# Kernel optimization log

Measured on AMD Instinct MI355X. Metric: run time of the kernel, lower is better.

## Reference

```python
import jax, jax.numpy as jnp
import numpy as np


def setup_inputs() -> dict:
    key = jax.random.key(0)
    k1, k2 = jax.random.split(key)
    N, M, D = 8192, 8192, 512
    x = jax.random.normal(k1, (N, D), dtype=jnp.float32)
    y = jax.random.normal(k2, (M, D), dtype=jnp.float32)
    gamma = jnp.float32(1.0)
    return {"x": x, "y": y, "gamma": gamma}


def reference(x, y, gamma):
    # k(x, y) = exp(-gamma * ||x - y||^2)
    x = x.reshape(-1, x.shape[-1])
    y = y.reshape(-1, y.shape[-1])
    x_sq = jnp.sum(x * x, axis=-1)  # [N]
    y_sq = jnp.sum(y * y, axis=-1)  # [M]
    cross = x @ y.T                  # [N, M]
    sq_dist = x_sq[:, None] + y_sq[None, :] - 2.0 * cross
    sq_dist = jnp.maximum(sq_dist, 0.0)  # guard tiny negative roundoff
    return jnp.exp(-gamma * sq_dist)
```

## Files before the change

kernel.cpp:

```cpp
#include <hip/hip_runtime.h>
#include <hip/hip_bf16.h>

typedef unsigned short u16;
typedef __attribute__((ext_vector_type(8))) short bf16x8;
typedef __attribute__((ext_vector_type(4))) float f32x4;

typedef const __attribute__((address_space(1))) void gvoid_t;
typedef __attribute__((address_space(3))) void lvoid_t;

__device__ __forceinline__ void gload_lds16(const void* g, void* l) {
  __builtin_amdgcn_global_load_lds((gvoid_t*)g, (lvoid_t*)l, 16, 0, 0);
}

__device__ __forceinline__ u16 f2bf(float f) {
  union { float f; unsigned u; } a;
  a.f = f;
  unsigned r = (a.u + 0x7FFFu + ((a.u >> 16) & 1u)) >> 16;
  return (u16)r;
}

__global__ __launch_bounds__(128) void rbf_prep(
    const float* __restrict__ x, const float* __restrict__ y,
    u16* __restrict__ xb, u16* __restrict__ yb,
    float* __restrict__ xsq, float* __restrict__ ysq,
    int N, int M, int D) {
  int row = blockIdx.x;
  const float* src;
  u16* dst;
  float* sq;
  if (row < N) {
    src = x + (size_t)row * D;
    dst = xb + (size_t)row * D;
    sq = xsq + row;
  } else {
    int r = row - N;
    src = y + (size_t)r * D;
    dst = yb + (size_t)r * D;
    sq = ysq + r;
  }
  int t = threadIdx.x;
  float4 v = reinterpret_cast<const float4*>(src)[t];
  float s = v.x * v.x + v.y * v.y + v.z * v.z + v.w * v.w;
  ushort4 o;
  o.x = f2bf(v.x);
  o.y = f2bf(v.y);
  o.z = f2bf(v.z);
  o.w = f2bf(v.w);
  reinterpret_cast<ushort4*>(dst)[t] = o;
  #pragma unroll
  for (int off = 32; off > 0; off >>= 1) s += __shfl_down(s, off, 64);
  __shared__ float red[2];
  if ((t & 63) == 0) red[t >> 6] = s;
  __syncthreads();
  if (t == 0) sq[0] = red[0] + red[1];
}

#define BM 256
#define BN 256
#define BK 64

__global__ __launch_bounds__(512, 2) void rbf_gemm(
    const u16* __restrict__ xb, const u16* __restrict__ yb,
    const float* __restrict__ xsq, const float* __restrict__ ysq,
    const float* __restrict__ gptr, float* __restrict__ out,
    int N, int M, int D) {
  __shared__ u16 lds[2][2][BM * BK];

  int nwg = gridDim.x;
  int bid = blockIdx.x;
  int cpx = nwg >> 3;
  int swz = (bid & 7) * cpx + (bid >> 3);
  int nbn = M / BN;
  int brow = (swz / nbn) * BM;
  int bcol = (swz % nbn) * BN;

  int tid = threadIdx.x;
  int w = tid >> 6;
  int lane = tid & 63;
  int wm = w >> 2;
  int wn = w & 3;
  int fr = lane & 15;
  int fq = lane >> 4;

  int srow = lane >> 3;
  int scol = ((lane & 7) * 8) ^ ((lane >= 32) ? 16 : 0);
  const u16* xsrc = xb + (size_t)(brow + w * 32 + srow) * D + scol;
  const u16* ysrc = yb + (size_t)(bcol + w * 32 + srow) * D + scol;
  int sdst = w * 4 * 512;

  int cswz = (fr & 4) ? 16 : 0;
  int colx0 = (fq * 8) ^ cswz;
  int colx1 = (32 + fq * 8) ^ cswz;
  int aoff0 = (wm * 128 + fr) * 64 + colx0;
  int aoff1 = (wm * 128 + fr) * 64 + colx1;
  int boff0 = (wn * 64 + fr) * 64 + colx0;
  int boff1 = (wn * 64 + fr) * 64 + colx1;

  f32x4 acc[8][4];
  #pragma unroll
  for (int m = 0; m < 8; ++m)
    #pragma unroll
    for (int n = 0; n < 4; ++n)
      acc[m][n] = (f32x4){0.f, 0.f, 0.f, 0.f};

  auto stage = [&](int kt, int b) {
    const u16* xs = xsrc + kt * 64;
    const u16* ys = ysrc + kt * 64;
    u16* la = &lds[b][0][sdst];
    u16* lb = &lds[b][1][sdst];
    #pragma unroll
    for (int i = 0; i < 4; ++i)
      gload_lds16(xs + (size_t)i * 8 * D, la + i * 512);
    #pragma unroll
    for (int i = 0; i < 4; ++i)
      gload_lds16(ys + (size_t)i * 8 * D, lb + i * 512);
  };

#define PHASE(MH, NH, RA, RB)                                                  \
  {                                                                            \
    if (RA) {                                                                  \
      _Pragma("unroll") for (int mi = 0; mi < 4; ++mi) {                       \
        af[mi][0] = *(const bf16x8*)&A[aoff0 + (MH * 4 + mi) * 1024];          \
        af[mi][1] = *(const bf16x8*)&A[aoff1 + (MH * 4 + mi) * 1024];          \
      }                                                                        \
    }                                                                          \
    if (RB) {                                                                  \
      _Pragma("unroll") for (int ni = 0; ni < 2; ++ni) {                       \
        bf[ni][0] = *(const bf16x8*)&B[boff0 + (NH * 2 + ni) * 1024];          \
        bf[ni][1] = *(const bf16x8*)&B[boff1 + (NH * 2 + ni) * 1024];          \
      }                                                                        \
    }                                                                          \
    __builtin_amdgcn_s_setprio(1);                                             \
    _Pragma("unroll") for (int mi = 0; mi < 4; ++mi)                           \
      _Pragma("unroll") for (int ni = 0; ni < 2; ++ni) {                       \
        acc[MH * 4 + mi][NH * 2 + ni] =                                        \
            __builtin_amdgcn_mfma_f32_16x16x32_bf16(                           \
                af[mi][0], bf[ni][0], acc[MH * 4 + mi][NH * 2 + ni], 0, 0, 0); \
        acc[MH * 4 + mi][NH * 2 + ni] =                                        \
            __builtin_amdgcn_mfma_f32_16x16x32_bf16(                           \
                af[mi][1], bf[ni][1], acc[MH * 4 + mi][NH * 2 + ni], 0, 0, 0); \
      }                                                                        \
    __builtin_amdgcn_s_setprio(0);                                             \
  }

  int nkt = D >> 6;
  stage(0, 0);
  stage(1, 1);
  for (int t = 0; t < nkt; ++t) {
    int b = t & 1;
    if (t + 1 < nkt)
      asm volatile("s_waitcnt vmcnt(8)" ::: "memory");
    else
      asm volatile("s_waitcnt vmcnt(0)" ::: "memory");
    __builtin_amdgcn_sched_barrier(0);
    __builtin_amdgcn_s_barrier();
    __builtin_amdgcn_sched_barrier(0);

    const u16* A = &lds[b][0][0];
    const u16* B = &lds[b][1][0];
    bf16x8 af[4][2], bf[2][2];

    PHASE(0, 0, true, true);
    __builtin_amdgcn_s_barrier();
    PHASE(0, 1, false, true);
    __builtin_amdgcn_s_barrier();
    PHASE(1, 1, true, false);
    __builtin_amdgcn_s_barrier();
    PHASE(1, 0, false, true);

    asm volatile("s_waitcnt lgkmcnt(0)" ::: "memory");
    __builtin_amdgcn_sched_barrier(0);
    __builtin_amdgcn_s_barrier();
    __builtin_amdgcn_sched_barrier(0);
    if (t + 2 < nkt) stage(t + 2, b);
  }
#undef PHASE

  float gamma = gptr[0];
  float ysv[4];
  #pragma unroll
  for (int n = 0; n < 4; ++n) ysv[n] = ysq[bcol + wn * 64 + n * 16 + fr];
  #pragma unroll
  for (int m = 0; m < 8; ++m) {
    #pragma unroll
    for (int r = 0; r < 4; ++r) {
      int i = brow + wm * 128 + m * 16 + fq * 4 + r;
      float xs = xsq[i];
      size_t ro = (size_t)i * M;
      #pragma unroll
      for (int n = 0; n < 4; ++n) {
        int j = bcol + wn * 64 + n * 16 + fr;
        float d2 = fmaxf(xs + ysv[n] - 2.0f * acc[m][n][r], 0.0f);
        out[ro + j] = __expf(-gamma * d2);
      }
    }
  }
}

__global__ __launch_bounds__(256) void rbf_naive(
    const float* __restrict__ x, const float* __restrict__ y,
    const float* __restrict__ gptr, float* __restrict__ out,
    int N, int M, int D) {
  __shared__ float xs[16][17];
  __shared__ float ys[16][17];
  int nbn = M / 16;
  int brow = (blockIdx.x / nbn) * 16;
  int bcol = (blockIdx.x % nbn) * 16;
  int ti = threadIdx.x >> 4, tj = threadIdx.x & 15;
  float dacc = 0.f, xacc = 0.f, yacc = 0.f;
  for (int k0 = 0; k0 < D; k0 += 16) {
    xs[ti][tj] = x[(size_t)(brow + ti) * D + k0 + tj];
    ys[ti][tj] = y[(size_t)(bcol + ti) * D + k0 + tj];
    __syncthreads();
    #pragma unroll
    for (int kk = 0; kk < 16; ++kk) {
      float xv = xs[ti][kk], yv = ys[tj][kk];
      dacc += xv * yv;
      xacc += xv * xv;
      yacc += yv * yv;
    }
    __syncthreads();
  }
  float gamma = gptr[0];
  float d2 = fmaxf(xacc + yacc - 2.f * dacc, 0.f);
  out[(size_t)(brow + ti) * M + (bcol + tj)] = __expf(-gamma * d2);
}

extern "C" void kernel_launch(void* const* d_in, const int* in_sizes, int n_in,
                              void* d_out, int out_size, void* d_ws,
                              size_t ws_size, hipStream_t stream) {
  const float* x = (const float*)d_in[0];
  const float* y = (const float*)d_in[1];
  const float* g = (const float*)d_in[2];
  float* out = (float*)d_out;

  const int D = 512;
  const int N = in_sizes[0] / D;
  const int M = in_sizes[1] / D;

  size_t need = (size_t)(N + M) * D * sizeof(u16) + (size_t)(N + M) * sizeof(float);
  bool shapes_ok = (N % BM == 0) && (M % BN == 0) && (D % BK == 0) && (D / BK >= 2);

  if (ws_size >= need && shapes_ok) {
    u16* xb = (u16*)d_ws;
    u16* yb = xb + (size_t)N * D;
    float* xsq = (float*)(yb + (size_t)M * D);
    float* ysq = xsq + N;

    rbf_prep<<<N + M, 128, 0, stream>>>(x, y, xb, yb, xsq, ysq, N, M, D);
    int nwg = (N / BM) * (M / BN);
    rbf_gemm<<<nwg, 512, 0, stream>>>(xb, yb, xsq, ysq, g, out, N, M, D);
  } else {
    rbf_naive<<<(N / 16) * (M / 16), 256, 0, stream>>>(x, y, g, out, N, M, D);
  }
}
```

Measured before the change: 124.5 us.

## Use full XOR LDS swizzle and transposed MFMA operands for vectorized stores

Changes the LDS layout swizzle from a two-way XOR to a full 8-way XOR keyed on row, to remove bank conflicts on the fragment reads. Swaps the A and B operands of the MFMA so each lane's accumulator holds four consecutive output columns instead of four rows. The epilogue then writes float4 stores per lane and loads ysq as float4, replacing scattered scalar stores. The gain depends on the epilogue store cost and LDS conflicts, and the operand swap has to stay consistent with the new indexing.

New measurement: 128.1 us. 1.03x slower.

```diff
diff --git a/kernel.cpp b/kernel.cpp
--- a/kernel.cpp
+++ b/kernel.cpp
@@ -83,14 +83,14 @@
   int fq = lane >> 4;
 
   int srow = lane >> 3;
-  int scol = ((lane & 7) * 8) ^ ((lane >= 32) ? 16 : 0);
+  int scol = ((lane & 7) ^ (srow & 7)) * 8;
   const u16* xsrc = xb + (size_t)(brow + w * 32 + srow) * D + scol;
   const u16* ysrc = yb + (size_t)(bcol + w * 32 + srow) * D + scol;
-  int sdst = w * 4 * 512;
-
-  int cswz = (fr & 4) ? 16 : 0;
-  int colx0 = (fq * 8) ^ cswz;
-  int colx1 = (32 + fq * 8) ^ cswz;
+  int sdst = w * 2048;
+
+  int cxor = (fr & 7) * 8;
+  int colx0 = (fq * 8) ^ cxor;
+  int colx1 = (32 + fq * 8) ^ cxor;
   int aoff0 = (wm * 128 + fr) * 64 + colx0;
   int aoff1 = (wm * 128 + fr) * 64 + colx1;
   int boff0 = (wn * 64 + fr) * 64 + colx0;
@@ -135,10 +135,10 @@
       _Pragma("unroll") for (int ni = 0; ni < 2; ++ni) {                       \
         acc[MH * 4 + mi][NH * 2 + ni] =                                        \
             __builtin_amdgcn_mfma_f32_16x16x32_bf16(                           \
-                af[mi][0], bf[ni][0], acc[MH * 4 + mi][NH * 2 + ni], 0, 0, 0); \
+                bf[ni][0], af[mi][0], acc[MH * 4 + mi][NH * 2 + ni], 0, 0, 0); \
         acc[MH * 4 + mi][NH * 2 + ni] =                                        \
             __builtin_amdgcn_mfma_f32_16x16x32_bf16(                           \
-                af[mi][1], bf[ni][1], acc[MH * 4 + mi][NH * 2 + ni], 0, 0, 0); \
+                bf[ni][1], af[mi][1], acc[MH * 4 + mi][NH * 2 + ni], 0, 0, 0); \
       }                                                                        \
     __builtin_amdgcn_s_setprio(0);                                             \
   }
@@ -177,22 +177,21 @@
 #undef PHASE
 
   float gamma = gptr[0];
-  float ysv[4];
-  #pragma unroll
-  for (int n = 0; n < 4; ++n) ysv[n] = ysq[bcol + wn * 64 + n * 16 + fr];
   #pragma unroll
   for (int m = 0; m < 8; ++m) {
-    #pragma unroll
-    for (int r = 0; r < 4; ++r) {
-      int i = brow + wm * 128 + m * 16 + fq * 4 + r;
-      float xs = xsq[i];
-      size_t ro = (size_t)i * M;
-      #pragma unroll
-      for (int n = 0; n < 4; ++n) {
-        int j = bcol + wn * 64 + n * 16 + fr;
-        float d2 = fmaxf(xs + ysv[n] - 2.0f * acc[m][n][r], 0.0f);
-        out[ro + j] = __expf(-gamma * d2);
-      }
+    int i = brow + wm * 128 + m * 16 + fr;
+    float xs = xsq[i];
+    size_t ro = (size_t)i * M;
+    #pragma unroll
+    for (int n = 0; n < 4; ++n) {
+      int jb = bcol + wn * 64 + n * 16 + fq * 4;
+      float4 ys4 = *reinterpret_cast<const float4*>(&ysq[jb]);
+      float4 e;
+      e.x = __expf(-gamma * fmaxf(xs + ys4.x - 2.0f * acc[m][n][0], 0.0f));
+      e.y = __expf(-gamma * fmaxf(xs + ys4.y - 2.0f * acc[m][n][1], 0.0f));
+      e.z = __expf(-gamma * fmaxf(xs + ys4.z - 2.0f * acc[m][n][2], 0.0f));
+      e.w = __expf(-gamma * fmaxf(xs + ys4.w - 2.0f * acc[m][n][3], 0.0f));
+      *reinterpret_cast<float4*>(&out[ro + jb]) = e;
     }
   }
 }
```
